# Optimization experiments

Measured on AMD Instinct MI355X. Metric: run time of the kernel, lower is better.

Reference implementation:

```python
import jax, jax.numpy as jnp
import numpy as np

N_NODES = 50000
N_EDGES = 800000
D_FEAT = 128
EMBED_DIM = 128
NUM_HEADS = 8
HEAD_DIM = EMBED_DIM // NUM_HEADS


def mish(x):
    return x * jnp.tanh(jax.nn.softplus(x))


def setup_inputs() -> dict:
    key = jax.random.key(0)
    ks = jax.random.split(key, 8)
    nodes = jax.random.normal(ks[0], (N_NODES, D_FEAT), dtype=jnp.float32)
    senders = jax.random.randint(ks[1], (N_EDGES,), 0, N_NODES, dtype=jnp.int32)
    receivers = jax.random.randint(ks[2], (N_EDGES,), 0, N_NODES, dtype=jnp.int32)
    s = 1.0 / np.sqrt(D_FEAT)
    Ws_k = jax.random.normal(ks[3], (D_FEAT, NUM_HEADS, HEAD_DIM), dtype=jnp.float32) * s
    Ws_b = jnp.zeros((NUM_HEADS, HEAD_DIM), dtype=jnp.float32)
    Wr_k = jax.random.normal(ks[4], (D_FEAT, NUM_HEADS, HEAD_DIM), dtype=jnp.float32) * s
    Wr_b = jnp.zeros((NUM_HEADS, HEAD_DIM), dtype=jnp.float32)
    attn_k = jax.random.normal(ks[5], (HEAD_DIM, 1), dtype=jnp.float32) / np.sqrt(HEAD_DIM)
    attn_b = jnp.zeros((1,), dtype=jnp.float32)
    return {"nodes": nodes, "senders": senders, "receivers": receivers,
            "Ws_k": Ws_k, "Ws_b": Ws_b, "Wr_k": Wr_k, "Wr_b": Wr_b,
            "attn_k": attn_k, "attn_b": attn_b}


def reference(nodes, senders, receivers, Ws_k, Ws_b, Wr_k, Wr_b, attn_k, attn_b):
    # gather endpoint features along edges
    sent = nodes[senders]        # [E, F]
    recv = nodes[receivers]      # [E, F]
    # edge messages: W_s(sent) -> [E, H, D]
    edges = jnp.einsum('ef,fhd->ehd', sent, Ws_k) + Ws_b
    # attention logits: Dense(1)(mish(edges + W_r(recv))) -> [E, H, 1]
    x = mish(edges + jnp.einsum('ef,fhd->ehd', recv, Wr_k) + Wr_b)
    logits = jnp.einsum('ehd,do->eho', x, attn_k) + attn_b  # [E, H, 1]
    # segment softmax over incoming edges of each receiver node
    seg_max = jax.ops.segment_max(logits, receivers, num_segments=N_NODES)  # [N, H, 1]
    unnorm = jnp.exp(logits - seg_max[receivers])
    denom = jax.ops.segment_sum(unnorm, receivers, num_segments=N_NODES)   # [N, H, 1]
    weights = unnorm / denom[receivers]                                     # [E, H, 1]
    # attention-weighted scatter-add into receiver nodes
    agg = jax.ops.segment_sum(edges * weights, receivers, num_segments=N_NODES)  # [N, H, D]
    # node update: concat heads
    return agg.reshape(N_NODES, NUM_HEADS * HEAD_DIM)
```

## Files before the change

### kernel.cpp

```cpp
#include <hip/hip_runtime.h>

#define N_NODES 50000
#define N_EDGES 800000
#define HEADS 8
#define HD 16
#define F 128
#define RPB 16
#define RPT 8
#define SCAN_B 1024
#define NB1 ((N_NODES + SCAN_B - 1) / SCAN_B)
#define TILE 8

__device__ __forceinline__ float mish_x(float x) {
    const float ex = __expf(x);
    const float z  = 1.0f + ex;
    const float zz = fmaf(z, z, 1.0f);
    const float r  = __builtin_amdgcn_rcpf(zz);
    return fmaf(-2.0f * x, r, x);
}

__device__ __forceinline__ float head8_sum(float x) {
    int v;
    v = __builtin_amdgcn_update_dpp(0, __float_as_int(x), 0xB1, 0xF, 0xF, true);
    x += __int_as_float(v);
    v = __builtin_amdgcn_update_dpp(0, __float_as_int(x), 0x4E, 0xF, 0xF, true);
    x += __int_as_float(v);
    v = __builtin_amdgcn_update_dpp(0, __float_as_int(x), 0x141, 0xF, 0xF, true);
    x += __int_as_float(v);
    return x;
}

__global__ __launch_bounds__(256) void k_proj_hist(
        const float* __restrict__ nodes,
        const float* __restrict__ Ws, const float* __restrict__ Wsb,
        const float* __restrict__ Wr, const float* __restrict__ Wrb,
        const int* __restrict__ receivers, int* __restrict__ counts,
        float* __restrict__ Ps, float* __restrict__ Pr) {
    __shared__ float rows[RPB][F];
    const int tid  = (int)threadIdx.x;
    const int o    = tid & 127;
    const int half = tid >> 7;
    const int r0   = blockIdx.x * RPB;

    atomicAdd(counts + receivers[blockIdx.x * 256 + tid], 1);

    for (int i = half; i < RPB; i += 2)
        rows[i][o] = nodes[(r0 + i) * F + o];
    __syncthreads();

    float accs[RPT], accr[RPT];
    const float bs = Wsb[o], br = Wrb[o];
    #pragma unroll
    for (int i = 0; i < RPT; ++i) { accs[i] = bs; accr[i] = br; }

    const int rbase = half * RPT;
    for (int f4 = 0; f4 < F / 4; ++f4) {
        const int f = f4 << 2;
        float4 ws4, wr4;
        ws4.x = Ws[(f + 0) * F + o];  ws4.y = Ws[(f + 1) * F + o];
        ws4.z = Ws[(f + 2) * F + o];  ws4.w = Ws[(f + 3) * F + o];
        wr4.x = Wr[(f + 0) * F + o];  wr4.y = Wr[(f + 1) * F + o];
        wr4.z = Wr[(f + 2) * F + o];  wr4.w = Wr[(f + 3) * F + o];
        #pragma unroll
        for (int i = 0; i < RPT; ++i) {
            const float4 rv = *(const float4*)(&rows[rbase + i][f]);
            accs[i] = fmaf(rv.x, ws4.x, accs[i]);
            accs[i] = fmaf(rv.y, ws4.y, accs[i]);
            accs[i] = fmaf(rv.z, ws4.z, accs[i]);
            accs[i] = fmaf(rv.w, ws4.w, accs[i]);
            accr[i] = fmaf(rv.x, wr4.x, accr[i]);
            accr[i] = fmaf(rv.y, wr4.y, accr[i]);
            accr[i] = fmaf(rv.z, wr4.z, accr[i]);
            accr[i] = fmaf(rv.w, wr4.w, accr[i]);
        }
    }
    #pragma unroll
    for (int i = 0; i < RPT; ++i) {
        Ps[(r0 + rbase + i) * F + o] = accs[i];
        Pr[(r0 + rbase + i) * F + o] = accr[i];
    }
}

__global__ __launch_bounds__(1024) void k_scan1(
        const int* __restrict__ counts, int* __restrict__ starts,
        int* __restrict__ partials) {
    __shared__ int buf[SCAN_B];
    const int i = blockIdx.x * SCAN_B + threadIdx.x;
    const int v = (i < N_NODES) ? counts[i] : 0;
    buf[threadIdx.x] = v;
    __syncthreads();
    for (int off = 1; off < SCAN_B; off <<= 1) {
        const int t = (threadIdx.x >= (unsigned)off) ? buf[threadIdx.x - off] : 0;
        __syncthreads();
        buf[threadIdx.x] += t;
        __syncthreads();
    }
    if (i < N_NODES) starts[i] = buf[threadIdx.x] - v;
    if (threadIdx.x == SCAN_B - 1) partials[blockIdx.x] = buf[SCAN_B - 1];
}

__global__ __launch_bounds__(256) void k_fill(
        const int* __restrict__ senders, const int* __restrict__ receivers,
        const int* __restrict__ starts, const int* __restrict__ partials,
        int* __restrict__ cursor, int* __restrict__ slist) {
    __shared__ int off_lds[NB1];
    if (threadIdx.x < 64) {
        const int j = (int)threadIdx.x;
        const int v = (j < NB1) ? partials[j] : 0;
        int incl = v;
        #pragma unroll
        for (int d = 1; d < 64; d <<= 1) {
            const int u = __shfl_up(incl, d);
            if (j >= d) incl += u;
        }
        if (j < NB1) off_lds[j] = incl - v;
    }
    __syncthreads();
    const int e = blockIdx.x * 256 + (int)threadIdx.x;
    const int r = receivers[e];
    const int pos = atomicAdd(cursor + r, 1);
    slist[starts[r] + off_lds[r >> 10] + pos] = senders[e];
}

__global__ __launch_bounds__(256) void k_agg_fused(
        const int* __restrict__ starts, const int* __restrict__ counts,
        const int* __restrict__ partials, const int* __restrict__ slist,
        const float* __restrict__ Ps, const float* __restrict__ Pr,
        const float* __restrict__ attn_k, float* __restrict__ out) {
    const int lane = (int)threadIdx.x & 63;
    const int n = __builtin_amdgcn_readfirstlane(
                      blockIdx.x * 4 + ((int)threadIdx.x >> 6));
    const int d0 = lane << 1;

    const int sb = n >> 10;
    int v = (lane < sb) ? partials[lane] : 0;
    v += __shfl_xor(v, 1);  v += __shfl_xor(v, 2);  v += __shfl_xor(v, 4);
    v += __shfl_xor(v, 8);  v += __shfl_xor(v, 16); v += __shfl_xor(v, 32);

    const int e0 = starts[n] + v;
    const int e1 = e0 + counts[n];
    const float2 pr2 = *(const float2*)(Pr + (size_t)n * F + d0);
    const float2 ak2 = *(const float2*)(attn_k + (d0 & 15));

    float den = 0.0f, ax = 0.0f, ay = 0.0f;

    if (e1 > e0) {
        float2 cur[TILE], nxt[TILE];
        #pragma unroll
        for (int k = 0; k < TILE; ++k) {
            const int idx = (e0 + k < e1) ? e0 + k : e1 - 1;
            cur[k] = *(const float2*)(Ps + (size_t)slist[idx] * F + d0);
        }
        for (int i = e0; i < e1; i += TILE) {
            const bool more = (i + TILE) < e1;
            if (more) {
                #pragma unroll
                for (int k = 0; k < TILE; ++k) {
                    const int idx = (i + TILE + k < e1) ? i + TILE + k : e1 - 1;
                    nxt[k] = *(const float2*)(Ps + (size_t)slist[idx] * F + d0);
                }
            }
            #pragma unroll
            for (int k = 0; k < TILE; ++k) {
                const float mi = mish_x(cur[k].x + pr2.x) * ak2.x
                               + mish_x(cur[k].y + pr2.y) * ak2.y;
                const float s = head8_sum(mi);
                const float w = (i + k < e1) ? __expf(s) : 0.0f;
                den += w;
                ax = fmaf(w, cur[k].x, ax);
                ay = fmaf(w, cur[k].y, ay);
            }
            if (more) {
                #pragma unroll
                for (int k = 0; k < TILE; ++k) cur[k] = nxt[k];
            }
        }
    }
    const float inv = __builtin_amdgcn_rcpf(den);
    float2 o2;
    o2.x = (den > 0.0f) ? ax * inv : 0.0f;
    o2.y = (den > 0.0f) ? ay * inv : 0.0f;
    *(float2*)(out + (size_t)n * F + d0) = o2;
}

extern "C" void kernel_launch(void* const* d_in, const int* in_sizes, int n_in,
                              void* d_out, int out_size, void* d_ws, size_t ws_size,
                              hipStream_t stream) {
    const float* nodes     = (const float*)d_in[0];
    const int*   senders   = (const int*)  d_in[1];
    const int*   receivers = (const int*)  d_in[2];
    const float* Wsk       = (const float*)d_in[3];
    const float* Wsb       = (const float*)d_in[4];
    const float* Wrk       = (const float*)d_in[5];
    const float* Wrb       = (const float*)d_in[6];
    const float* attnk     = (const float*)d_in[7];
    float* out = (float*)d_out;

    float* Ps       = (float*)d_ws;
    float* Pr       = Ps + (size_t)N_NODES * F;
    int*   slist    = (int*)(Pr + (size_t)N_NODES * F);
    int*   counts   = slist + N_EDGES;
    int*   cursor   = counts + N_NODES;
    int*   starts   = cursor + N_NODES;
    int*   partials = starts + N_NODES + 1;

    hipMemsetAsync(counts, 0, 2 * N_NODES * sizeof(int), stream);

    k_proj_hist<<<N_NODES / RPB, 256, 0, stream>>>(nodes, Wsk, Wsb, Wrk, Wrb,
                                                   receivers, counts, Ps, Pr);
    k_scan1<<<NB1, SCAN_B, 0, stream>>>(counts, starts, partials);
    k_fill<<<N_EDGES / 256, 256, 0, stream>>>(senders, receivers, starts,
                                              partials, cursor, slist);
    k_agg_fused<<<N_NODES / 4, 256, 0, stream>>>(starts, counts, partials,
                                                 slist, Ps, Pr, attnk, out);
}
```

Before: 266.8 us.

## Record histogram atomic return slots to drop cursor atomics in fill

The histogram pass now stores the value returned by each edge's atomicAdd as that edge's slot within its receiver segment. The fill kernel then uses the stored slot instead of doing a second atomic on a cursor array, and the cursor memset goes away. The projection kernel also processes 32 rows per block, with 16 rows per thread, to cover two edges per thread, and adds bounds checks for the last partial block. The trade-offs are an extra 3.2MB slot array to write and read and doubled per-thread accumulator registers in the projection kernel, which may reduce occupancy.

```diff
diff --git a/kernel.cpp b/kernel.cpp
--- a/kernel.cpp
+++ b/kernel.cpp
@@ -5,8 +5,9 @@
 #define HEADS 8
 #define HD 16
 #define F 128
-#define RPB 16
-#define RPT 8
+#define RPB 32
+#define RPT 16
+#define PROJ_B ((N_NODES + RPB - 1) / RPB)
 #define SCAN_B 1024
 #define NB1 ((N_NODES + SCAN_B - 1) / SCAN_B)
 #define TILE 8
@@ -35,6 +36,7 @@
         const float* __restrict__ Ws, const float* __restrict__ Wsb,
         const float* __restrict__ Wr, const float* __restrict__ Wrb,
         const int* __restrict__ receivers, int* __restrict__ counts,
+        int* __restrict__ slot,
         float* __restrict__ Ps, float* __restrict__ Pr) {
     __shared__ float rows[RPB][F];
     const int tid  = (int)threadIdx.x;
@@ -42,10 +44,14 @@
     const int half = tid >> 7;
     const int r0   = blockIdx.x * RPB;
 
-    atomicAdd(counts + receivers[blockIdx.x * 256 + tid], 1);
-
-    for (int i = half; i < RPB; i += 2)
-        rows[i][o] = nodes[(r0 + i) * F + o];
+    const int e = blockIdx.x * 512 + tid;
+    if (e < N_EDGES)       slot[e]       = atomicAdd(counts + receivers[e], 1);
+    if (e + 256 < N_EDGES) slot[e + 256] = atomicAdd(counts + receivers[e + 256], 1);
+
+    for (int i = half; i < RPB; i += 2) {
+        const int rr = r0 + i;
+        rows[i][o] = (rr < N_NODES) ? nodes[rr * F + o] : 0.0f;
+    }
     __syncthreads();
 
     float accs[RPT], accr[RPT];
@@ -76,8 +82,11 @@
     }
     #pragma unroll
     for (int i = 0; i < RPT; ++i) {
-        Ps[(r0 + rbase + i) * F + o] = accs[i];
-        Pr[(r0 + rbase + i) * F + o] = accr[i];
+        const int rr = r0 + rbase + i;
+        if (rr < N_NODES) {
+            Ps[rr * F + o] = accs[i];
+            Pr[rr * F + o] = accr[i];
+        }
     }
 }
 
@@ -102,7 +111,7 @@
 __global__ __launch_bounds__(256) void k_fill(
         const int* __restrict__ senders, const int* __restrict__ receivers,
         const int* __restrict__ starts, const int* __restrict__ partials,
-        int* __restrict__ cursor, int* __restrict__ slist) {
+        const int* __restrict__ slot, int* __restrict__ slist) {
     __shared__ int off_lds[NB1];
     if (threadIdx.x < 64) {
         const int j = (int)threadIdx.x;
@@ -118,8 +127,7 @@
     __syncthreads();
     const int e = blockIdx.x * 256 + (int)threadIdx.x;
     const int r = receivers[e];
-    const int pos = atomicAdd(cursor + r, 1);
-    slist[starts[r] + off_lds[r >> 10] + pos] = senders[e];
+    slist[starts[r] + off_lds[r >> 10] + slot[e]] = senders[e];
 }
 
 __global__ __launch_bounds__(256) void k_agg_fused(
@@ -199,18 +207,18 @@
     float* Ps       = (float*)d_ws;
     float* Pr       = Ps + (size_t)N_NODES * F;
     int*   slist    = (int*)(Pr + (size_t)N_NODES * F);
-    int*   counts   = slist + N_EDGES;
-    int*   cursor   = counts + N_NODES;
-    int*   starts   = cursor + N_NODES;
+    int*   slot     = slist + N_EDGES;
+    int*   counts   = slot + N_EDGES;
+    int*   starts   = counts + N_NODES;
     int*   partials = starts + N_NODES + 1;
 
-    hipMemsetAsync(counts, 0, 2 * N_NODES * sizeof(int), stream);
-
-    k_proj_hist<<<N_NODES / RPB, 256, 0, stream>>>(nodes, Wsk, Wsb, Wrk, Wrb,
-                                                   receivers, counts, Ps, Pr);
+    hipMemsetAsync(counts, 0, N_NODES * sizeof(int), stream);
+
+    k_proj_hist<<<PROJ_B, 256, 0, stream>>>(nodes, Wsk, Wsb, Wrk, Wrb,
+                                            receivers, counts, slot, Ps, Pr);
     k_scan1<<<NB1, SCAN_B, 0, stream>>>(counts, starts, partials);
     k_fill<<<N_EDGES / 256, 256, 0, stream>>>(senders, receivers, starts,
-                                              partials, cursor, slist);
+                                              partials, slot, slist);
     k_agg_fused<<<N_NODES / 4, 256, 0, stream>>>(starts, counts, partials,
                                                  slist, Ps, Pr, attnk, out);
 }
```

Measured after the change: 260.3 us. 2.4% less time.
